# Kernel optimization log

Measured on AMD Instinct MI355X. Metric: run time of the kernel, lower is better.

## Reference

```python
import jax, jax.numpy as jnp
import numpy as np

DIM = 96
D_STATE = 16
EXPAND = 2
D_INNER = EXPAND * DIM
DT_RANK = (DIM + 15) // 16  # 6
B, H, W = 2, 64, 64
K = 4  # scan directions


def _ln(x, w, b, eps=1e-5):
    mu = x.mean(-1, keepdims=True)
    var = x.var(-1, keepdims=True)
    return (x - mu) / jnp.sqrt(var + eps) * w + b


def setup_inputs() -> dict:
    key = jax.random.key(0)
    ks = jax.random.split(key, 10)
    f = jnp.float32
    x = jax.random.normal(ks[0], (B, H, W, DIM), dtype=f)
    y = jax.random.normal(ks[1], (B, H, W, DIM), dtype=f)
    inp = {
        'x': x,
        'y': y,
        'ln_w': jnp.ones((DIM,), f),
        'ln_b': jnp.zeros((DIM,), f),
        'in_proj_w': jax.random.normal(ks[2], (2 * D_INNER, DIM), f) * 0.05,
        'conv_w': jax.random.normal(ks[3], (D_INNER, 1, 3, 3), f) * 0.1,
        'conv_b': jnp.zeros((D_INNER,), f),
        'x_proj_w': jax.random.normal(ks[4], (K, DT_RANK + 2 * D_STATE, D_INNER), f) * 0.05,
        'dt_w': jax.random.normal(ks[5], (K, D_INNER, DT_RANK), f) * 0.1,
        'dt_b': jax.random.normal(ks[6], (K, D_INNER), f) * 0.1,
        'A_log': jnp.broadcast_to(jnp.log(jnp.arange(1, D_STATE + 1, dtype=f)), (K, D_INNER, D_STATE)),
        'Ds': jnp.ones((K, D_INNER), f),
        'out_norm_w': jnp.ones((D_INNER,), f),
        'out_norm_b': jnp.zeros((D_INNER,), f),
        'out_proj_w': jax.random.normal(ks[7], (DIM, D_INNER), f) * 0.05,
    }
    return inp


def _fwd(x, y, ln_w, ln_b, in_proj_w, conv_w, conv_b, x_proj_w, dt_w, dt_b,
         A_log, Ds, out_norm_w, out_norm_b, out_proj_w):
    Bsz, Hh, Ww, C = x.shape
    Din = conv_w.shape[0]
    N = A_log.shape[-1]
    R = dt_w.shape[-1]
    L = Hh * Ww

    diff = jnp.abs(x - y)                       # TemporalSpectrumBlock abs-diff
    h = _ln(diff, ln_w, ln_b)                   # VSSBlock ln_1
    xz = h @ in_proj_w.T                        # (B,H,W,2*Din)
    xm, z = jnp.split(xz, 2, axis=-1)
    xm = xm.transpose(0, 3, 1, 2)               # (B,Din,H,W)
    xm = jax.lax.conv_general_dilated(
        xm, conv_w, (1, 1), 'SAME', feature_group_count=Din,
        dimension_numbers=('NCHW', 'OIHW', 'NCHW')) + conv_b[None, :, None, None]
    xm = jax.nn.silu(xm)

    # 4-directional sequences (B,4,Din,L)
    x0 = xm.reshape(Bsz, Din, L)
    x1 = xm.transpose(0, 1, 3, 2).reshape(Bsz, Din, L)
    xs = jnp.stack([x0, x1], axis=1)
    xs = jnp.concatenate([xs, jnp.flip(xs, axis=-1)], axis=1)

    x_dbl = jnp.einsum('bkdl,kcd->bkcl', xs, x_proj_w)
    dts, Bs, Cs = jnp.split(x_dbl, [R, R + N], axis=2)   # (B,4,R,L),(B,4,N,L),(B,4,N,L)
    dts = jnp.einsum('bkrl,kdr->bkdl', dts, dt_w)
    delta = jax.nn.softplus(dts + dt_b[None, :, :, None])  # (B,4,Din,L)

    A = -jnp.exp(A_log)                                    # (4,Din,N)
    dA = jnp.exp(delta[..., None] * A[None, :, :, None, :])          # (B,4,Din,L,N)
    dBu = delta[..., None] * Bs.transpose(0, 1, 3, 2)[:, :, None] * xs[..., None]

    dA_t = dA.transpose(3, 0, 1, 2, 4)    # (L,B,4,Din,N)
    dBu_t = dBu.transpose(3, 0, 1, 2, 4)
    C_t = Cs.transpose(3, 0, 1, 2)        # (L,B,4,N)
    h0 = jnp.zeros((Bsz, 4, Din, N), dtype=x.dtype)

    def step(hc, inp):
        a, bu, c = inp
        hc = a * hc + bu
        yv = jnp.einsum('bkdn,bkn->bkd', hc, c)
        return hc, yv

    _, ys = jax.lax.scan(step, h0, (dA_t, dBu_t, C_t))    # (L,B,4,Din)
    ys = ys.transpose(1, 2, 3, 0)                          # (B,4,Din,L)
    out_y = ys + Ds[None, :, :, None] * xs

    inv_y = jnp.flip(out_y[:, 2:4], axis=-1)
    wh_y = out_y[:, 1].reshape(Bsz, Din, Ww, Hh).transpose(0, 1, 3, 2).reshape(Bsz, Din, L)
    invwh_y = inv_y[:, 1].reshape(Bsz, Din, Ww, Hh).transpose(0, 1, 3, 2).reshape(Bsz, Din, L)
    yc = out_y[:, 0] + inv_y[:, 0] + wh_y + invwh_y        # (B,Din,L)
    yc = yc.transpose(0, 2, 1).reshape(Bsz, Hh, Ww, Din)

    yn = _ln(yc, out_norm_w, out_norm_b)
    out = (yn * jax.nn.silu(z)) @ out_proj_w.T
    return diff + out                                      # residual around the block


def reference(x, y, ln_w, ln_b, in_proj_w, conv_w, conv_b, x_proj_w, dt_w, dt_b,
              A_log, Ds, out_norm_w, out_norm_b, out_proj_w):
    return _fwd(x, y, ln_w, ln_b, in_proj_w, conv_w, conv_b, x_proj_w, dt_w, dt_b,
                A_log, Ds, out_norm_w, out_norm_b, out_proj_w)
```

## Files before the change

kernel.cpp:

```cpp
#include <hip/hip_runtime.h>
#include <math.h>

#define DIMC 96
#define DIN  192
#define NST  16
#define RNK  6
#define KD   4
#define HH   64
#define WWD  64
#define LL   4096
#define BB   2
#define NC   256
#define CH   16
#define CPK  48

__device__ __forceinline__ int pos_of(int k, int l) {
    int t = ((l & 63) << 6) | (l >> 6);
    switch (k) {
        case 0: return l;
        case 1: return t;
        case 2: return LL - 1 - l;
        default: return ((((LL-1-l) & 63) << 6) | ((LL-1-l) >> 6));
    }
}

__device__ __forceinline__ float silu_f(float v) {
    return v / (1.f + __expf(-v));
}

__global__ __launch_bounds__(256) void k0_prep(
    const float* __restrict__ Win, const float* __restrict__ Wout,
    const float* __restrict__ xpw,
    float* __restrict__ WinT, float* __restrict__ WoutT, float* __restrict__ wT3)
{
    int idx = blockIdx.x*256 + threadIdx.x;
    int stride = gridDim.x*256;
    for (int i = idx; i < 96*384; i += stride) {
        int j = i / 384, o = i - j*384;
        WinT[i] = Win[o*96 + j];
    }
    for (int i = idx; i < 192*96; i += stride) {
        int j = i / 96, o = i - j*96;
        WoutT[i] = Wout[o*192 + j];
    }
    for (int i = idx; i < KD*192*CPK; i += stride) {
        int kk = i / (192*CPK); int rem = i - kk*192*CPK;
        int j = rem / CPK, c = rem - j*CPK;
        float v = 0.f;
        if (c < 16)       v = xpw[((size_t)kk*(RNK+2*NST) + RNK + c)*DIN + j];
        else if (c < 32)  v = xpw[((size_t)kk*(RNK+2*NST) + RNK + NST + (c-16))*DIN + j];
        else if (c < 38)  v = xpw[((size_t)kk*(RNK+2*NST) + (c-32))*DIN + j];
        wT3[i] = v;
    }
}

__global__ __launch_bounds__(1024) void k1_ln_inproj(
    const float* __restrict__ x, const float* __restrict__ y,
    const float* __restrict__ lnw, const float* __restrict__ lnb,
    const float* __restrict__ WinT,
    float* __restrict__ diff, float* __restrict__ xm, float* __restrict__ zbuf)
{
    __shared__ float hT[96*65];
    __shared__ float ps1[16*64], ps2[16*64];
    __shared__ float mus[64], rss[64];
    int t = threadIdx.x;
    int ptile = blockIdx.x >> 1, cgrp = blockIdx.x & 1;
    int p0 = ptile*64;

    #pragma unroll
    for (int s = 0; s < 6; s++) {
        int i = t + 1024*s;
        float v = fabsf(x[(size_t)p0*96 + i] - y[(size_t)p0*96 + i]);
        if (cgrp == 0) diff[(size_t)p0*96 + i] = v;
        int pos = i / 96, ch = i - pos*96;
        hT[ch*65 + pos] = v;
    }
    __syncthreads();
    {
        int pos = t & 63, part = t >> 6;
        float s1 = 0.f, s2 = 0.f;
        #pragma unroll
        for (int m = 0; m < 6; m++) {
            float v = hT[(part*6 + m)*65 + pos];
            s1 += v; s2 += v*v;
        }
        ps1[part*64 + pos] = s1; ps2[part*64 + pos] = s2;
    }
    __syncthreads();
    if (t < 64) {
        float S1 = 0.f, S2 = 0.f;
        #pragma unroll
        for (int i = 0; i < 16; i++) { S1 += ps1[i*64 + t]; S2 += ps2[i*64 + t]; }
        float mu = S1 * (1.f/96.f);
        float var = S2 * (1.f/96.f) - mu*mu;
        mus[t] = mu; rss[t] = rsqrtf(var + 1e-5f);
    }
    __syncthreads();
    #pragma unroll
    for (int s = 0; s < 6; s++) {
        int i = t + 1024*s;
        int pos = i / 96, ch = i - pos*96;
        hT[ch*65 + pos] = (hT[ch*65 + pos] - mus[pos]) * rss[pos] * lnw[ch] + lnb[ch];
    }
    __syncthreads();

    int w = __builtin_amdgcn_readfirstlane(t >> 6);
    int lane = t & 63;
    int c0 = cgrp*192 + w*12;
    const float* wp = WinT + c0;
    float acc[12];
    #pragma unroll
    for (int cc = 0; cc < 12; cc++) acc[cc] = 0.f;
    #pragma unroll 2
    for (int j = 0; j < 96; j++) {
        float u = hT[j*65 + lane];
        const float* wrow = wp + j*384;
        #pragma unroll
        for (int cc = 0; cc < 12; cc++) acc[cc] += u * wrow[cc];
    }
    size_t p = (size_t)(p0 + lane);
    float* dst = (c0 < 192) ? (xm + p*192 + c0) : (zbuf + p*192 + (c0 - 192));
    #pragma unroll
    for (int q = 0; q < 3; q++)
        *(float4*)&dst[4*q] = make_float4(acc[4*q], acc[4*q+1], acc[4*q+2], acc[4*q+3]);
}

__global__ __launch_bounds__(192) void k2_conv(
    const float* __restrict__ xm, const float* __restrict__ cw,
    const float* __restrict__ cb, float* __restrict__ xconv)
{
    int p = blockIdx.x;
    int d = threadIdx.x;
    int b = p >> 12;
    int l = p & (LL - 1);
    int hh = l >> 6, ww = l & 63;
    float acc = cb[d];
    const float* wd = cw + d*9;
    #pragma unroll
    for (int di = -1; di <= 1; di++) {
        int h2 = hh + di;
        if ((unsigned)h2 < HH) {
            #pragma unroll
            for (int dj = -1; dj <= 1; dj++) {
                int w2 = ww + dj;
                if ((unsigned)w2 < WWD)
                    acc += wd[(di+1)*3 + (dj+1)] * xm[((size_t)b*LL + h2*WWD + w2)*DIN + d];
            }
        }
    }
    xconv[(size_t)p*DIN + d] = silu_f(acc);
}

__global__ __launch_bounds__(512) void k3_xproj(
    const float* __restrict__ xconv, const float* __restrict__ wT3,
    float* __restrict__ XDK)
{
    __shared__ float uT[192*65];
    int t = threadIdx.x;
    int ptile = blockIdx.x >> 1, wgrp = blockIdx.x & 1;
    int p0 = ptile*64;

    #pragma unroll
    for (int s = 0; s < 24; s++) {
        int i = t + 512*s;
        int pos = i / 192, ch = i - pos*192;
        uT[ch*65 + pos] = xconv[(size_t)(p0 + pos)*192 + ch];
    }
    __syncthreads();

    int w = __builtin_amdgcn_readfirstlane(t >> 6);
    int slot = wgrp*8 + w;
    int k = slot >> 2, cq = slot & 3;
    int lane = t & 63;
    int c0 = cq*12;
    const float* wp = wT3 + (size_t)k*192*CPK + c0;
    float acc[12];
    #pragma unroll
    for (int cc = 0; cc < 12; cc++) acc[cc] = 0.f;
    #pragma unroll 2
    for (int j = 0; j < 192; j++) {
        float u = uT[j*65 + lane];
        const float* wrow = wp + j*CPK;
        #pragma unroll
        for (int cc = 0; cc < 12; cc++) acc[cc] += u * wrow[cc];
    }
    int p = p0 + lane;
    int b = p >> 12;
    int s = p & (LL - 1);
    int ts = ((s & 63) << 6) | (s >> 6);
    int l;
    switch (k) {
        case 0: l = s; break;
        case 1: l = ts; break;
        case 2: l = LL - 1 - s; break;
        default: l = LL - 1 - ts; break;
    }
    float* dst = XDK + ((size_t)(b*KD + k)*LL + l)*CPK + c0;
    #pragma unroll
    for (int q = 0; q < 3; q++)
        *(float4*)&dst[4*q] = make_float4(acc[4*q], acc[4*q+1], acc[4*q+2], acc[4*q+3]);
}

__global__ __launch_bounds__(192) void k4_scanA(
    const float* __restrict__ xconv, const float* __restrict__ XDK,
    const float* __restrict__ dtw, const float* __restrict__ dtb,
    const float* __restrict__ A_log,
    float* __restrict__ Sarr, float* __restrict__ Q)
{
    int blk = blockIdx.x;
    int c  = blk & (NC - 1);
    int bk = blk >> 8;
    int k  = bk & 3;
    int b  = bk >> 2;
    int d  = threadIdx.x;
    float dw[RNK];
    #pragma unroll
    for (int r = 0; r < RNK; r++) dw[r] = dtw[((size_t)k*DIN + d)*RNK + r];
    float bias = dtb[k*DIN + d];
    float A[NST];
    #pragma unroll
    for (int n = 0; n < NST; n++) A[n] = -__expf(A_log[((size_t)k*DIN + d)*NST + n]);
    bool fastA = true;
    #pragma unroll
    for (int n = 1; n < NST; n++)
        fastA = fastA && (fabsf(A[n] - (float)(n+1)*A[0]) <= 1e-4f*(float)(n+1));

    float h[NST];
    #pragma unroll
    for (int n = 0; n < NST; n++) h[n] = 0.f;
    float S = 0.f;

    size_t rb = ((size_t)bk*LL + c*CH)*CPK;
    if (fastA) {
        #pragma unroll 2
        for (int step = 0; step < CH; step++) {
            const float* rec = XDK + rb + step*CPK;
            float dl = bias;
            #pragma unroll
            for (int r = 0; r < RNK; r++) dl += rec[32 + r] * dw[r];
            dl = (dl > 20.f) ? dl : __logf(1.f + __expf(dl));
            int l = c*CH + step;
            float uu = xconv[((size_t)b*LL + pos_of(k, l))*DIN + d];
            float du = dl * uu;
            S += dl;
            float e1 = __expf(dl * A[0]);
            float a = e1;
            #pragma unroll
            for (int n = 0; n < NST; n++) {
                h[n] = a*h[n] + du*rec[n];
                a *= e1;
            }
        }
    } else {
        #pragma unroll 2
        for (int step = 0; step < CH; step++) {
            const float* rec = XDK + rb + step*CPK;
            float dl = bias;
            #pragma unroll
            for (int r = 0; r < RNK; r++) dl += rec[32 + r] * dw[r];
            dl = (dl > 20.f) ? dl : __logf(1.f + __expf(dl));
            int l = c*CH + step;
            float uu = xconv[((size_t)b*LL + pos_of(k, l))*DIN + d];
            float du = dl * uu;
            S += dl;
            #pragma unroll
            for (int n = 0; n < NST; n++) {
                float a = __expf(dl * A[n]);
                h[n] = a*h[n] + du*rec[n];
            }
        }
    }
    Sarr[(size_t)blk*DIN + d] = S;
    size_t qb = (size_t)blk*NST*DIN + d;
    #pragma unroll
    for (int n = 0; n < NST; n++) Q[qb + n*DIN] = h[n];
}

__global__ __launch_bounds__(256) void k5_scanB(
    const float* __restrict__ A_log, const float* __restrict__ Sarr,
    float* __restrict__ Q)
{
    int idx = blockIdx.x*256 + threadIdx.x;
    if (idx >= BB*KD*NST*DIN) return;
    int d = idx % DIN;
    int rest = idx / DIN;
    int n = rest % NST; rest /= NST;
    int k = rest & 3;
    int b = rest >> 2;
    int bk = b*KD + k;
    float A = -__expf(A_log[((size_t)k*DIN + d)*NST + n]);
    size_t qstride = (size_t)NST*DIN;
    size_t qbase = (size_t)bk*NC*qstride + n*DIN + d;
    size_t sbase = (size_t)bk*NC*DIN + d;
    float h = 0.f;
    #pragma unroll 4
    for (int c = 0; c < NC; c++) {
        float s = Sarr[sbase + c*DIN];
        float q = Q[qbase + c*qstride];
        Q[qbase + c*qstride] = h;
        h = __expf(A*s)*h + q;
    }
}

__global__ __launch_bounds__(192) void k6_scanC(
    const float* __restrict__ xconv, const float* __restrict__ XDK,
    const float* __restrict__ dtw, const float* __restrict__ dtb,
    const float* __restrict__ A_log, const float* __restrict__ Ds,
    const float* __restrict__ Q, float* __restrict__ outy)
{
    int blk = blockIdx.x;
    int c  = blk & (NC - 1);
    int bk = blk >> 8;
    int k  = bk & 3;
    int b  = bk >> 2;
    int d  = threadIdx.x;
    float dw[RNK];
    #pragma unroll
    for (int r = 0; r < RNK; r++) dw[r] = dtw[((size_t)k*DIN + d)*RNK + r];
    float bias = dtb[k*DIN + d];
    float A[NST];
    #pragma unroll
    for (int n = 0; n < NST; n++) A[n] = -__expf(A_log[((size_t)k*DIN + d)*NST + n]);
    bool fastA = true;
    #pragma unroll
    for (int n = 1; n < NST; n++)
        fastA = fastA && (fabsf(A[n] - (float)(n+1)*A[0]) <= 1e-4f*(float)(n+1));
    float h[NST];
    size_t qb = (size_t)blk*NST*DIN + d;
    #pragma unroll
    for (int n = 0; n < NST; n++) h[n] = Q[qb + n*DIN];
    float Dv = Ds[k*DIN + d];

    size_t rb = ((size_t)bk*LL + c*CH)*CPK;
    if (fastA) {
        #pragma unroll 2
        for (int step = 0; step < CH; step++) {
            const float* rec = XDK + rb + step*CPK;
            float dl = bias;
            #pragma unroll
            for (int r = 0; r < RNK; r++) dl += rec[32 + r] * dw[r];
            dl = (dl > 20.f) ? dl : __logf(1.f + __expf(dl));
            int l = c*CH + step;
            int sp = pos_of(k, l);
            float uu = xconv[((size_t)b*LL + sp)*DIN + d];
            float du = dl * uu;
            float e1 = __expf(dl * A[0]);
            float a = e1;
            float yv = 0.f;
            #pragma unroll
            for (int n = 0; n < NST; n++) {
                h[n] = a*h[n] + du*rec[n];
                yv += h[n] * rec[16 + n];
                a *= e1;
            }
            outy[((size_t)bk*LL + sp)*DIN + d] = yv + Dv*uu;
        }
    } else {
        #pragma unroll 2
        for (int step = 0; step < CH; step++) {
            const float* rec = XDK + rb + step*CPK;
            float dl = bias;
            #pragma unroll
            for (int r = 0; r < RNK; r++) dl += rec[32 + r] * dw[r];
            dl = (dl > 20.f) ? dl : __logf(1.f + __expf(dl));
            int l = c*CH + step;
            int sp = pos_of(k, l);
            float uu = xconv[((size_t)b*LL + sp)*DIN + d];
            float du = dl * uu;
            float yv = 0.f;
            #pragma unroll
            for (int n = 0; n < NST; n++) {
                float a = __expf(dl * A[n]);
                h[n] = a*h[n] + du*rec[n];
                yv += h[n] * rec[16 + n];
            }
            outy[((size_t)bk*LL + sp)*DIN + d] = yv + Dv*uu;
        }
    }
}

__global__ __launch_bounds__(256) void k7_out(
    const float* __restrict__ outy, const float* __restrict__ zbuf,
    const float* __restrict__ diff, const float* __restrict__ onw,
    const float* __restrict__ onb, const float* __restrict__ WoutT,
    float* __restrict__ out)
{
    __shared__ float gT[192*65];
    __shared__ float ps1[4*64], ps2[4*64];
    __shared__ float mus[64], rss[64];
    int t = threadIdx.x;
    int ptile = blockIdx.x >> 1, chalf = blockIdx.x & 1;
    int p0 = ptile*64;
    int b = p0 >> 12;
    int l0 = p0 & (LL - 1);
    const size_t seg = (size_t)LL*DIN;
    size_t base = ((size_t)(b*KD)*LL + l0)*DIN;

    #pragma unroll
    for (int s = 0; s < 48; s++) {
        int i = t + 256*s;
        float yc = outy[base + i] + outy[base + seg + i]
                 + outy[base + 2*seg + i] + outy[base + 3*seg + i];
        int pos = i / 192, ch = i - pos*192;
        gT[ch*65 + pos] = yc;
    }
    __syncthreads();
    {
        int pos = t & 63, part = t >> 6;
        float s1 = 0.f, s2 = 0.f;
        #pragma unroll
        for (int m = 0; m < 48; m++) {
            float v = gT[(part*48 + m)*65 + pos];
            s1 += v; s2 += v*v;
        }
        ps1[part*64 + pos] = s1; ps2[part*64 + pos] = s2;
    }
    __syncthreads();
    if (t < 64) {
        float S1 = ps1[t] + ps1[64+t] + ps1[128+t] + ps1[192+t];
        float S2 = ps2[t] + ps2[64+t] + ps2[128+t] + ps2[192+t];
        float mu = S1 * (1.f/192.f);
        float var = S2 * (1.f/192.f) - mu*mu;
        mus[t] = mu; rss[t] = rsqrtf(var + 1e-5f);
    }
    __syncthreads();
    #pragma unroll
    for (int s = 0; s < 48; s++) {
        int i = t + 256*s;
        int pos = i / 192, ch = i - pos*192;
        float v = gT[ch*65 + pos];
        float yn = (v - mus[pos]) * rss[pos] * onw[ch] + onb[ch];
        float z = zbuf[(size_t)p0*DIN + i];
        gT[ch*65 + pos] = yn * silu_f(z);
    }
    __syncthreads();

    int w = __builtin_amdgcn_readfirstlane(t >> 6);
    int lane = t & 63;
    int c0 = chalf*48 + w*12;
    const float* wp = WoutT + c0;
    float acc[12];
    #pragma unroll
    for (int cc = 0; cc < 12; cc++) acc[cc] = 0.f;
    #pragma unroll 2
    for (int j = 0; j < 192; j++) {
        float u = gT[j*65 + lane];
        const float* wrow = wp + j*96;
        #pragma unroll
        for (int cc = 0; cc < 12; cc++) acc[cc] += u * wrow[cc];
    }
    size_t p = (size_t)(p0 + lane);
    #pragma unroll
    for (int q = 0; q < 3; q++) {
        float4 dv = *(const float4*)&diff[p*96 + c0 + 4*q];
        *(float4*)&out[p*96 + c0 + 4*q] =
            make_float4(acc[4*q] + dv.x, acc[4*q+1] + dv.y, acc[4*q+2] + dv.z, acc[4*q+3] + dv.w);
    }
}

extern "C" void kernel_launch(void* const* d_in, const int* in_sizes, int n_in,
                              void* d_out, int out_size, void* d_ws, size_t ws_size,
                              hipStream_t stream)
{
    const float* x       = (const float*)d_in[0];
    const float* y       = (const float*)d_in[1];
    const float* ln_w    = (const float*)d_in[2];
    const float* ln_b    = (const float*)d_in[3];
    const float* in_proj = (const float*)d_in[4];
    const float* conv_w  = (const float*)d_in[5];
    const float* conv_b  = (const float*)d_in[6];
    const float* x_proj  = (const float*)d_in[7];
    const float* dt_w    = (const float*)d_in[8];
    const float* dt_b    = (const float*)d_in[9];
    const float* A_log   = (const float*)d_in[10];
    const float* Ds      = (const float*)d_in[11];
    const float* onw     = (const float*)d_in[12];
    const float* onb     = (const float*)d_in[13];
    const float* out_w   = (const float*)d_in[14];
    float* out = (float*)d_out;

    float* ws    = (float*)d_ws;
    float* diff  = ws;
    float* zbuf  = diff  + 786432;
    float* xm    = zbuf  + 1572864;
    float* xconv = xm    + 1572864;
    float* XDK   = xconv + 1572864;
    float* outy  = XDK   + 1572864;
    float* Qbuf  = outy  + 6291456;
    float* Sarr  = Qbuf  + 6291456;
    float* WinT  = Sarr  + 393216;
    float* WoutT = WinT  + 36864;
    float* wT3   = WoutT + 18432;

    const int BL = BB * LL;

    hipLaunchKernelGGL(k0_prep, dim3(144), dim3(256), 0, stream,
                       in_proj, out_w, x_proj, WinT, WoutT, wT3);
    hipLaunchKernelGGL(k1_ln_inproj, dim3(BL/64*2), dim3(1024), 0, stream,
                       x, y, ln_w, ln_b, WinT, diff, xm, zbuf);
    hipLaunchKernelGGL(k2_conv, dim3(BL), dim3(DIN), 0, stream,
                       xm, conv_w, conv_b, xconv);
    hipLaunchKernelGGL(k3_xproj, dim3(BL/64*2), dim3(512), 0, stream,
                       xconv, wT3, XDK);
    hipLaunchKernelGGL(k4_scanA, dim3(BB*KD*NC), dim3(DIN), 0, stream,
                       xconv, XDK, dt_w, dt_b, A_log, Sarr, Qbuf);
    hipLaunchKernelGGL(k5_scanB, dim3((BB*KD*NST*DIN + 255)/256), dim3(256), 0, stream,
                       A_log, Sarr, Qbuf);
    hipLaunchKernelGGL(k6_scanC, dim3(BB*KD*NC), dim3(DIN), 0, stream,
                       xconv, XDK, dt_w, dt_b, A_log, Ds, Qbuf, outy);
    hipLaunchKernelGGL(k7_out, dim3(BL/64*2), dim3(256), 0, stream,
                       outy, zbuf, diff, onw, onb, WoutT, out);
}
```

Measured before the change: 276.8 us.

## Split scan state dimension across two blocks and split output stage into two kernels

The chunk count is halved (CH 32, NC 128) and each chunk is handled by two blocks that each own 8 of the 16 state channels, keeping the total block count and the k5 chunk carry the same. Each half writes its partial y to a separate outy buffer, and the combine stage sums eight buffers. The output stage is split into a per-position LayerNorm/gate kernel and a GEMM kernel with quarter-width column tiles for more blocks. This cuts per-thread register state and work in the scans, but duplicates dt/softplus/exp work across the halves, doubles outy traffic, and adds an extra pass through gbuf.

```diff
diff --git a/kernel.cpp b/kernel.cpp
--- a/kernel.cpp
+++ b/kernel.cpp
@@ -10,8 +10,8 @@
 #define WWD  64
 #define LL   4096
 #define BB   2
-#define NC   256
-#define CH   16
+#define NC   128
+#define CH   32
 #define CPK  48
 
 __device__ __forceinline__ int pos_of(int k, int l) {
@@ -208,7 +208,8 @@
     float* __restrict__ Sarr, float* __restrict__ Q)
 {
     int blk = blockIdx.x;
-    int c  = blk & (NC - 1);
+    int nh = blk & 1;
+    int c  = (blk >> 1) & (NC - 1);
     int bk = blk >> 8;
     int k  = bk & 3;
     int b  = bk >> 2;
@@ -217,24 +218,27 @@
     #pragma unroll
     for (int r = 0; r < RNK; r++) dw[r] = dtw[((size_t)k*DIN + d)*RNK + r];
     float bias = dtb[k*DIN + d];
-    float A[NST];
-    #pragma unroll
-    for (int n = 0; n < NST; n++) A[n] = -__expf(A_log[((size_t)k*DIN + d)*NST + n]);
+    float A0 = -__expf(A_log[((size_t)k*DIN + d)*NST]);
+    float Ah[8];
+    #pragma unroll
+    for (int g = 0; g < 8; g++) Ah[g] = -__expf(A_log[((size_t)k*DIN + d)*NST + nh*8 + g]);
     bool fastA = true;
     #pragma unroll
-    for (int n = 1; n < NST; n++)
-        fastA = fastA && (fabsf(A[n] - (float)(n+1)*A[0]) <= 1e-4f*(float)(n+1));
-
-    float h[NST];
-    #pragma unroll
-    for (int n = 0; n < NST; n++) h[n] = 0.f;
+    for (int g = 0; g < 8; g++) {
+        float m = (float)(nh*8 + g + 1);
+        fastA = fastA && (fabsf(Ah[g] - m*A0) <= 1e-4f*m);
+    }
+
+    float h[8];
+    #pragma unroll
+    for (int g = 0; g < 8; g++) h[g] = 0.f;
     float S = 0.f;
 
-    size_t rb = ((size_t)bk*LL + c*CH)*CPK;
+    size_t rb = ((size_t)bk*LL + c*CH);
     if (fastA) {
         #pragma unroll 2
         for (int step = 0; step < CH; step++) {
-            const float* rec = XDK + rb + step*CPK;
+            const float* rec = XDK + (rb + step)*CPK;
             float dl = bias;
             #pragma unroll
             for (int r = 0; r < RNK; r++) dl += rec[32 + r] * dw[r];
@@ -243,18 +247,22 @@
             float uu = xconv[((size_t)b*LL + pos_of(k, l))*DIN + d];
             float du = dl * uu;
             S += dl;
-            float e1 = __expf(dl * A[0]);
-            float a = e1;
-            #pragma unroll
-            for (int n = 0; n < NST; n++) {
-                h[n] = a*h[n] + du*rec[n];
-                a *= e1;
+            float e1 = __expf(dl * A0);
+            float E2 = e1*e1, E4 = E2*E2, E8 = E4*E4;
+            float a[8];
+            a[0]=e1; a[1]=E2; a[2]=E2*e1; a[3]=E4; a[4]=E4*e1; a[5]=E4*E2; a[6]=E4*E2*e1; a[7]=E8;
+            if (nh) {
+                #pragma unroll
+                for (int g = 0; g < 8; g++) a[g] *= E8;
             }
+            #pragma unroll
+            for (int g = 0; g < 8; g++)
+                h[g] = a[g]*h[g] + du*rec[nh*8 + g];
         }
     } else {
         #pragma unroll 2
         for (int step = 0; step < CH; step++) {
-            const float* rec = XDK + rb + step*CPK;
+            const float* rec = XDK + (rb + step)*CPK;
             float dl = bias;
             #pragma unroll
             for (int r = 0; r < RNK; r++) dl += rec[32 + r] * dw[r];
@@ -264,16 +272,16 @@
             float du = dl * uu;
             S += dl;
             #pragma unroll
-            for (int n = 0; n < NST; n++) {
-                float a = __expf(dl * A[n]);
-                h[n] = a*h[n] + du*rec[n];
+            for (int g = 0; g < 8; g++) {
+                float a = __expf(dl * Ah[g]);
+                h[g] = a*h[g] + du*rec[nh*8 + g];
             }
         }
     }
-    Sarr[(size_t)blk*DIN + d] = S;
-    size_t qb = (size_t)blk*NST*DIN + d;
-    #pragma unroll
-    for (int n = 0; n < NST; n++) Q[qb + n*DIN] = h[n];
+    if (nh == 0) Sarr[(size_t)(blk >> 1)*DIN + d] = S;
+    size_t qb = (size_t)(blk >> 1)*NST*DIN + nh*8*DIN + d;
+    #pragma unroll
+    for (int g = 0; g < 8; g++) Q[qb + g*DIN] = h[g];
 }
 
 __global__ __launch_bounds__(256) void k5_scanB(
@@ -306,10 +314,12 @@
     const float* __restrict__ xconv, const float* __restrict__ XDK,
     const float* __restrict__ dtw, const float* __restrict__ dtb,
     const float* __restrict__ A_log, const float* __restrict__ Ds,
-    const float* __restrict__ Q, float* __restrict__ outy)
+    const float* __restrict__ Q,
+    float* __restrict__ outy0, float* __restrict__ outy1)
 {
     int blk = blockIdx.x;
-    int c  = blk & (NC - 1);
+    int nh = blk & 1;
+    int c  = (blk >> 1) & (NC - 1);
     int bk = blk >> 8;
     int k  = bk & 3;
     int b  = bk >> 2;
@@ -318,24 +328,28 @@
     #pragma unroll
     for (int r = 0; r < RNK; r++) dw[r] = dtw[((size_t)k*DIN + d)*RNK + r];
     float bias = dtb[k*DIN + d];
-    float A[NST];
-    #pragma unroll
-    for (int n = 0; n < NST; n++) A[n] = -__expf(A_log[((size_t)k*DIN + d)*NST + n]);
+    float A0 = -__expf(A_log[((size_t)k*DIN + d)*NST]);
+    float Ah[8];
+    #pragma unroll
+    for (int g = 0; g < 8; g++) Ah[g] = -__expf(A_log[((size_t)k*DIN + d)*NST + nh*8 + g]);
     bool fastA = true;
     #pragma unroll
-    for (int n = 1; n < NST; n++)
-        fastA = fastA && (fabsf(A[n] - (float)(n+1)*A[0]) <= 1e-4f*(float)(n+1));
-    float h[NST];
-    size_t qb = (size_t)blk*NST*DIN + d;
-    #pragma unroll
-    for (int n = 0; n < NST; n++) h[n] = Q[qb + n*DIN];
+    for (int g = 0; g < 8; g++) {
+        float m = (float)(nh*8 + g + 1);
+        fastA = fastA && (fabsf(Ah[g] - m*A0) <= 1e-4f*m);
+    }
+    float h[8];
+    size_t qb = (size_t)(blk >> 1)*NST*DIN + nh*8*DIN + d;
+    #pragma unroll
+    for (int g = 0; g < 8; g++) h[g] = Q[qb + g*DIN];
     float Dv = Ds[k*DIN + d];
-
-    size_t rb = ((size_t)bk*LL + c*CH)*CPK;
+    float* oy = nh ? outy1 : outy0;
+
+    size_t rb = ((size_t)bk*LL + c*CH);
     if (fastA) {
         #pragma unroll 2
         for (int step = 0; step < CH; step++) {
-            const float* rec = XDK + rb + step*CPK;
+            const float* rec = XDK + (rb + step)*CPK;
             float dl = bias;
             #pragma unroll
             for (int r = 0; r < RNK; r++) dl += rec[32 + r] * dw[r];
@@ -344,21 +358,27 @@
             int sp = pos_of(k, l);
             float uu = xconv[((size_t)b*LL + sp)*DIN + d];
             float du = dl * uu;
-            float e1 = __expf(dl * A[0]);
-            float a = e1;
+            float e1 = __expf(dl * A0);
+            float E2 = e1*e1, E4 = E2*E2, E8 = E4*E4;
+            float a[8];
+            a[0]=e1; a[1]=E2; a[2]=E2*e1; a[3]=E4; a[4]=E4*e1; a[5]=E4*E2; a[6]=E4*E2*e1; a[7]=E8;
+            if (nh) {
+                #pragma unroll
+                for (int g = 0; g < 8; g++) a[g] *= E8;
+            }
             float yv = 0.f;
             #pragma unroll
-            for (int n = 0; n < NST; n++) {
-                h[n] = a*h[n] + du*rec[n];
-                yv += h[n] * rec[16 + n];
-                a *= e1;
+            for (int g = 0; g < 8; g++) {
+                h[g] = a[g]*h[g] + du*rec[nh*8 + g];
+                yv += h[g]*rec[16 + nh*8 + g];
             }
-            outy[((size_t)bk*LL + sp)*DIN + d] = yv + Dv*uu;
+            if (nh == 0) yv += Dv*uu;
+            oy[((size_t)bk*LL + sp)*DIN + d] = yv;
         }
     } else {
         #pragma unroll 2
         for (int step = 0; step < CH; step++) {
-            const float* rec = XDK + rb + step*CPK;
+            const float* rec = XDK + (rb + step)*CPK;
             float dl = bias;
             #pragma unroll
             for (int r = 0; r < RNK; r++) dl += rec[32 + r] * dw[r];
@@ -369,92 +389,90 @@
             float du = dl * uu;
             float yv = 0.f;
             #pragma unroll
-            for (int n = 0; n < NST; n++) {
-                float a = __expf(dl * A[n]);
-                h[n] = a*h[n] + du*rec[n];
-                yv += h[n] * rec[16 + n];
+            for (int g = 0; g < 8; g++) {
+                float a = __expf(dl * Ah[g]);
+                h[g] = a*h[g] + du*rec[nh*8 + g];
+                yv += h[g]*rec[16 + nh*8 + g];
             }
-            outy[((size_t)bk*LL + sp)*DIN + d] = yv + Dv*uu;
+            if (nh == 0) yv += Dv*uu;
+            oy[((size_t)bk*LL + sp)*DIN + d] = yv;
         }
     }
 }
 
-__global__ __launch_bounds__(256) void k7_out(
-    const float* __restrict__ outy, const float* __restrict__ zbuf,
-    const float* __restrict__ diff, const float* __restrict__ onw,
-    const float* __restrict__ onb, const float* __restrict__ WoutT,
-    float* __restrict__ out)
-{
-    __shared__ float gT[192*65];
-    __shared__ float ps1[4*64], ps2[4*64];
-    __shared__ float mus[64], rss[64];
-    int t = threadIdx.x;
-    int ptile = blockIdx.x >> 1, chalf = blockIdx.x & 1;
-    int p0 = ptile*64;
-    int b = p0 >> 12;
-    int l0 = p0 & (LL - 1);
+__global__ __launch_bounds__(192) void k7a_comb(
+    const float* __restrict__ outy0, const float* __restrict__ outy1,
+    const float* __restrict__ zbuf, const float* __restrict__ onw,
+    const float* __restrict__ onb, float* __restrict__ gbuf)
+{
+    __shared__ float red1[3], red2[3];
+    __shared__ float s_mu, s_rs;
+    int p = blockIdx.x;
+    int d = threadIdx.x;
+    int b = p >> 12;
     const size_t seg = (size_t)LL*DIN;
-    size_t base = ((size_t)(b*KD)*LL + l0)*DIN;
-
-    #pragma unroll
-    for (int s = 0; s < 48; s++) {
-        int i = t + 256*s;
-        float yc = outy[base + i] + outy[base + seg + i]
-                 + outy[base + 2*seg + i] + outy[base + 3*seg + i];
-        int pos = i / 192, ch = i - pos*192;
-        gT[ch*65 + pos] = yc;
-    }
-    __syncthreads();
-    {
-        int pos = t & 63, part = t >> 6;
-        float s1 = 0.f, s2 = 0.f;
-        #pragma unroll
-        for (int m = 0; m < 48; m++) {
-            float v = gT[(part*48 + m)*65 + pos];
-            s1 += v; s2 += v*v;
-        }
-        ps1[part*64 + pos] = s1; ps2[part*64 + pos] = s2;
-    }
-    __syncthreads();
-    if (t < 64) {
-        float S1 = ps1[t] + ps1[64+t] + ps1[128+t] + ps1[192+t];
-        float S2 = ps2[t] + ps2[64+t] + ps2[128+t] + ps2[192+t];
+    size_t base = ((size_t)(b*KD)*LL + (p & (LL-1)))*DIN + d;
+
+    float yc = outy0[base] + outy0[base + seg] + outy0[base + 2*seg] + outy0[base + 3*seg]
+             + outy1[base] + outy1[base + seg] + outy1[base + 2*seg] + outy1[base + 3*seg];
+
+    float s1 = yc, s2 = yc*yc;
+    #pragma unroll
+    for (int off = 32; off > 0; off >>= 1) {
+        s1 += __shfl_down(s1, off);
+        s2 += __shfl_down(s2, off);
+    }
+    int wid = d >> 6, lane = d & 63;
+    if (lane == 0) { red1[wid] = s1; red2[wid] = s2; }
+    __syncthreads();
+    if (d == 0) {
+        float S1 = red1[0] + red1[1] + red1[2];
+        float S2 = red2[0] + red2[1] + red2[2];
         float mu = S1 * (1.f/192.f);
         float var = S2 * (1.f/192.f) - mu*mu;
-        mus[t] = mu; rss[t] = rsqrtf(var + 1e-5f);
-    }
-    __syncthreads();
+        s_mu = mu; s_rs = rsqrtf(var + 1e-5f);
+    }
+    __syncthreads();
+    float yn = (yc - s_mu) * s_rs * onw[d] + onb[d];
+    gbuf[(size_t)p*DIN + d] = yn * silu_f(zbuf[(size_t)p*DIN + d]);
+}
+
+__global__ __launch_bounds__(256) void k7b_gemm(
+    const float* __restrict__ gbuf, const float* __restrict__ diff,
+    const float* __restrict__ WoutT, float* __restrict__ out)
+{
+    __shared__ float gT[192*65];
+    int t = threadIdx.x;
+    int ptile = blockIdx.x >> 2, cq = blockIdx.x & 3;
+    int p0 = ptile*64;
+
     #pragma unroll
     for (int s = 0; s < 48; s++) {
         int i = t + 256*s;
         int pos = i / 192, ch = i - pos*192;
-        float v = gT[ch*65 + pos];
-        float yn = (v - mus[pos]) * rss[pos] * onw[ch] + onb[ch];
-        float z = zbuf[(size_t)p0*DIN + i];
-        gT[ch*65 + pos] = yn * silu_f(z);
+        gT[ch*65 + pos] = gbuf[(size_t)(p0 + pos)*192 + ch];
     }
     __syncthreads();
 
     int w = __builtin_amdgcn_readfirstlane(t >> 6);
     int lane = t & 63;
-    int c0 = chalf*48 + w*12;
+    int c0 = cq*24 + w*6;
     const float* wp = WoutT + c0;
-    float acc[12];
-    #pragma unroll
-    for (int cc = 0; cc < 12; cc++) acc[cc] = 0.f;
+    float acc[6];
+    #pragma unroll
+    for (int cc = 0; cc < 6; cc++) acc[cc] = 0.f;
     #pragma unroll 2
     for (int j = 0; j < 192; j++) {
         float u = gT[j*65 + lane];
         const float* wrow = wp + j*96;
         #pragma unroll
-        for (int cc = 0; cc < 12; cc++) acc[cc] += u * wrow[cc];
+        for (int cc = 0; cc < 6; cc++) acc[cc] += u * wrow[cc];
     }
     size_t p = (size_t)(p0 + lane);
     #pragma unroll
     for (int q = 0; q < 3; q++) {
-        float4 dv = *(const float4*)&diff[p*96 + c0 + 4*q];
-        *(float4*)&out[p*96 + c0 + 4*q] =
-            make_float4(acc[4*q] + dv.x, acc[4*q+1] + dv.y, acc[4*q+2] + dv.z, acc[4*q+3] + dv.w);
+        float2 dv = *(const float2*)&diff[p*96 + c0 + 2*q];
+        *(float2*)&out[p*96 + c0 + 2*q] = make_float2(acc[2*q] + dv.x, acc[2*q+1] + dv.y);
     }
 }
 
@@ -485,10 +503,12 @@
     float* xm    = zbuf  + 1572864;
     float* xconv = xm    + 1572864;
     float* XDK   = xconv + 1572864;
-    float* outy  = XDK   + 1572864;
-    float* Qbuf  = outy  + 6291456;
-    float* Sarr  = Qbuf  + 6291456;
-    float* WinT  = Sarr  + 393216;
+    float* outy0 = XDK   + 1572864;
+    float* outy1 = outy0 + 6291456;
+    float* Qbuf  = outy1 + 6291456;
+    float* Sarr  = Qbuf  + 3145728;
+    float* gbuf  = Sarr  + 196608;
+    float* WinT  = gbuf  + 1572864;
     float* WoutT = WinT  + 36864;
     float* wT3   = WoutT + 18432;
 
@@ -502,12 +522,14 @@
                        xm, conv_w, conv_b, xconv);
     hipLaunchKernelGGL(k3_xproj, dim3(BL/64*2), dim3(512), 0, stream,
                        xconv, wT3, XDK);
-    hipLaunchKernelGGL(k4_scanA, dim3(BB*KD*NC), dim3(DIN), 0, stream,
+    hipLaunchKernelGGL(k4_scanA, dim3(BB*KD*NC*2), dim3(DIN), 0, stream,
                        xconv, XDK, dt_w, dt_b, A_log, Sarr, Qbuf);
     hipLaunchKernelGGL(k5_scanB, dim3((BB*KD*NST*DIN + 255)/256), dim3(256), 0, stream,
                        A_log, Sarr, Qbuf);
-    hipLaunchKernelGGL(k6_scanC, dim3(BB*KD*NC), dim3(DIN), 0, stream,
-                       xconv, XDK, dt_w, dt_b, A_log, Ds, Qbuf, outy);
-    hipLaunchKernelGGL(k7_out, dim3(BL/64*2), dim3(256), 0, stream,
-                       outy, zbuf, diff, onw, onb, WoutT, out);
-}
+    hipLaunchKernelGGL(k6_scanC, dim3(BB*KD*NC*2), dim3(DIN), 0, stream,
+                       xconv, XDK, dt_w, dt_b, A_log, Ds, Qbuf, outy0, outy1);
+    hipLaunchKernelGGL(k7a_comb, dim3(BL), dim3(DIN), 0, stream,
+                       outy0, outy1, zbuf, onw, onb, gbuf);
+    hipLaunchKernelGGL(k7b_gemm, dim3(128*4), dim3(256), 0, stream,
+                       gbuf, diff, WoutT, out);
+}
```

Result: slower. 285.2 us (+3.0%).
